# Performance work log

Hardware: AMD Instinct MI355X
Metric: run time of the kernel (lower is better)

## Reference

```python
import jax, jax.numpy as jnp
import numpy as np

B, S, P, N = 256, 128, 100, 500
E, H, L, F = 256, 4, 2, 1024   # embed, heads, layers, ffn
V, U, I = 50000, 10000, 10000


def setup_inputs() -> dict:
    key = jax.random.key(0)
    ks = jax.random.split(key, 32)
    u = lambda k, shp: jax.random.uniform(k, shp, jnp.float32, -0.1, 0.1)
    n = lambda k, shp, s=0.02: jax.random.normal(k, shp, jnp.float32) * s
    inp = {
        'attr': jax.random.randint(ks[0], (B, S), 0, V),
        'attr_inds': jax.random.randint(ks[1], (B, S), 0, S),
        'attr_tf': jax.random.uniform(ks[2], (B, S), jnp.float32),
        'attr_feat': jax.random.normal(ks[3], (B, 13), jnp.float32),
        'attr_lens': jax.random.randint(ks[4], (B,), S // 2, S + 1).at[0].set(S),
        'attr_lens_user': jax.random.randint(ks[5], (B,), 0, S),
        'attr_lens_item': jax.random.randint(ks[6], (B,), 0, S),
        'user_ids': jax.random.randint(ks[7], (B,), 0, U),
        'item_ids': jax.random.randint(ks[8], (B,), 0, I),
        'pos_targets': jax.random.randint(ks[9], (B, P), 0, V),
        'pos_lens': jax.random.randint(ks[10], (B,), 1, P + 1).at[0].set(P),
        'neg_targets': jax.random.randint(ks[11], (B, N), 0, V),
        'neg_lens': jax.random.randint(ks[12], (B,), 1, N + 1).at[0].set(N),
        # parameters (init_uniform(-0.1,0.1) like f_init_weight)
        'attr_emb': u(ks[13], (V, E)),
        'user_emb': u(ks[14], (U, E)),
        'item_emb': u(ks[15], (I, E)),
        'out_emb': u(ks[16], (V, 3 * E)),
        'fw_W': n(ks[17], (1, 13), 0.1),
        'fw_b': jnp.zeros((1,), jnp.float32),
        'qkv_w': n(ks[18], (L, 3 * E, E)),
        'qkv_b': jnp.zeros((L, 3 * E), jnp.float32),
        'attn_out_w': n(ks[19], (L, E, E)),
        'attn_out_b': jnp.zeros((L, E), jnp.float32),
        'ln1_s': jnp.ones((L, E), jnp.float32),
        'ln1_b': jnp.zeros((L, E), jnp.float32),
        'ff1_w': n(ks[20], (L, F, E)),
        'ff1_b': jnp.zeros((L, F), jnp.float32),
        'ff2_w': n(ks[21], (L, E, F)),
        'ff2_b': jnp.zeros((L, E), jnp.float32),
        'ln2_s': jnp.ones((L, E), jnp.float32),
        'ln2_b': jnp.zeros((L, E), jnp.float32),
    }
    return inp


def _ln(x, s, b, eps=1e-5):
    m = jnp.mean(x, axis=-1, keepdims=True)
    v = jnp.mean(jnp.square(x - m), axis=-1, keepdims=True)
    return (x - m) * jax.lax.rsqrt(v + eps) * s + b


def _encoder_layer(x, pad, p):
    # PyTorch TransformerEncoderLayer (post-norm, relu, dropout=0/eval)
    b, s, e = x.shape
    hd = e // H
    qkv = x @ p['qkv_w'].T + p['qkv_b']                      # [B,S,3E]
    q, k, v = jnp.split(qkv, 3, axis=-1)
    q = q.reshape(b, s, H, hd)
    k = k.reshape(b, s, H, hd)
    v = v.reshape(b, s, H, hd)
    scores = jnp.einsum('bqhd,bkhd->bhqk', q, k) / jnp.sqrt(jnp.float32(hd))
    scores = scores + jnp.where(pad[:, None, None, :], -1e9, 0.0)
    a = jax.nn.softmax(scores, axis=-1)
    o = jnp.einsum('bhqk,bkhd->bqhd', a, v).reshape(b, s, e)
    o = o @ p['attn_out_w'].T + p['attn_out_b']
    x = _ln(x + o, p['ln1_s'], p['ln1_b'])
    h = jax.nn.relu(x @ p['ff1_w'].T + p['ff1_b'])
    h = h @ p['ff2_w'].T + p['ff2_b']
    return _ln(x + h, p['ln2_s'], p['ln2_b'])


def reference(attr, attr_inds, attr_tf, attr_feat, attr_lens, attr_lens_user,
              attr_lens_item, user_ids, item_ids, pos_targets, pos_lens,
              neg_targets, neg_lens, attr_emb, user_emb, item_emb, out_emb,
              fw_W, fw_b, qkv_w, qkv_b, attn_out_w, attn_out_b, ln1_s, ln1_b,
              ff1_w, ff1_b, ff2_w, ff2_b, ln2_s, ln2_b):
    b, s = attr.shape
    pos = jnp.arange(s)
    pad = pos[None, :] >= attr_lens[:, None]                 # True = padding
    x = attr_emb[attr]                                       # [B,S,E]
    for l in range(qkv_w.shape[0]):
        p = {'qkv_w': qkv_w[l], 'qkv_b': qkv_b[l],
             'attn_out_w': attn_out_w[l], 'attn_out_b': attn_out_b[l],
             'ln1_s': ln1_s[l], 'ln1_b': ln1_b[l],
             'ff1_w': ff1_w[l], 'ff1_b': ff1_b[l],
             'ff2_w': ff2_w[l], 'ff2_b': ff2_b[l],
             'ln2_s': ln2_s[l], 'ln2_b': ln2_b[l]}
        x = _encoder_layer(x, pad, p)
    # per-sample scalar user weight; vectorized ragged user/item tf weighting
    w_user = jax.nn.sigmoid(attr_feat @ fw_W.T + fw_b)[:, 0]           # [B]
    side = jnp.where(pos[None, :] < attr_lens_user[:, None],
                     w_user[:, None], 1.0 - w_user[:, None])           # [B,S]
    weight = attr_tf * side * (~pad)                                   # [B,S]
    attr_x = jnp.einsum('bs,bse->be', weight, x)                       # [B,E]
    output = jnp.concatenate([user_emb[user_ids], attr_x,
                              item_emb[item_ids]], axis=-1)            # [B,3E]
    pos_logits = jnp.einsum('bpe,be->bp', out_emb[pos_targets], output)
    neg_logits = jnp.einsum('bne,be->bn', out_emb[neg_targets], output)
    pos_valid = jnp.arange(pos_targets.shape[1])[None, :] < pos_lens[:, None]
    neg_valid = jnp.arange(neg_targets.shape[1])[None, :] < neg_lens[:, None]
    logits = jnp.concatenate([pos_logits, neg_logits], axis=-1)
    mask = jnp.concatenate([pos_valid, neg_valid], axis=-1)
    new_targets = jnp.concatenate([jnp.ones_like(pos_targets),
                                   jnp.zeros_like(neg_targets)], axis=1)
    new_targets = new_targets * mask.astype(new_targets.dtype)
    return logits, mask, new_targets
```

## Files before the change

### kernel.cpp

```cpp
#include <hip/hip_runtime.h>
#include <hip/hip_bf16.h>

typedef __bf16 bf16_t;
typedef __bf16 bf16x8 __attribute__((ext_vector_type(8)));
typedef __bf16 bf16x4 __attribute__((ext_vector_type(4)));
typedef float f32x4 __attribute__((ext_vector_type(4)));

#define B_ 256
#define S_ 128
#define E_ 256
#define H_ 4
#define HD_ 64
#define F_ 1024
#define TPOS_ 100
#define TNEG_ 500
#define TT_ 600
#define ROWS_ (B_ * S_)

__global__ __launch_bounds__(256) void cvtall_kernel(
        const float* __restrict__ sq, const float* __restrict__ sa,
        const float* __restrict__ s1, const float* __restrict__ s2,
        bf16_t* __restrict__ dq, bf16_t* __restrict__ da,
        bf16_t* __restrict__ d1, bf16_t* __restrict__ d2) {
    int i = blockIdx.x * 256 + threadIdx.x;
    if (i < 393216) { dq[i] = (bf16_t)sq[i]; }
    else if (i < 524288) { int j = i - 393216; da[j] = (bf16_t)sa[j]; }
    else if (i < 1048576) { int j = i - 524288; d1[j] = (bf16_t)s1[j]; }
    else { int j = i - 1048576; d2[j] = (bf16_t)s2[j]; }
}

__global__ __launch_bounds__(256) void embed_kernel(const int* __restrict__ attr,
        const float* __restrict__ emb, bf16_t* __restrict__ xb) {
    int row = blockIdx.x * 4 + (threadIdx.x >> 6);
    int lane = threadIdx.x & 63;
    int idx = attr[row];
    float4 v = reinterpret_cast<const float4*>(emb + (size_t)idx * E_)[lane];
    bf16x4 o; o[0] = (bf16_t)v.x; o[1] = (bf16_t)v.y; o[2] = (bf16_t)v.z; o[3] = (bf16_t)v.w;
    *reinterpret_cast<bf16x4*>(xb + (size_t)row * E_ + lane * 4) = o;
}

template<bool RELU>
__global__ __launch_bounds__(256) void gemm_kernel(
        const bf16_t* __restrict__ A, const bf16_t* __restrict__ W,
        const float* __restrict__ bias, bf16_t* __restrict__ outB, int M, int N, int K) {
    __shared__ bf16_t lA[2][128 * 32];
    __shared__ bf16_t lB[2][128 * 32];
    int tid = threadIdx.x;
    int wave = tid >> 6, lane = tid & 63;
    int wr = wave >> 1, wc = wave & 1;
    int mBase = blockIdx.y * 128;
    int nBase = blockIdx.x * 128;
    int r16 = lane & 15, kg = lane >> 4;

    int srow = wave * 16 + (lane >> 2);
    int scol = (lane & 3) * 8;
    const bf16_t* gA = A + (size_t)(mBase + srow) * K + scol;
    const bf16_t* gB = W + (size_t)(nBase + srow) * K + scol;
    int ldst = wave * 512;

    f32x4 acc[4][4] = {};

    #define STAGE(buf, k0) { \
        _Pragma("unroll") \
        for (int iss = 0; iss < 2; iss++) { \
            __builtin_amdgcn_global_load_lds( \
                (const __attribute__((address_space(1))) void*)(gA + (size_t)iss * 64 * K + (k0)), \
                (__attribute__((address_space(3))) void*)(&lA[buf][iss * 2048 + ldst]), 16, 0, 0); \
            __builtin_amdgcn_global_load_lds( \
                (const __attribute__((address_space(1))) void*)(gB + (size_t)iss * 64 * K + (k0)), \
                (__attribute__((address_space(3))) void*)(&lB[buf][iss * 2048 + ldst]), 16, 0, 0); \
        } }

    STAGE(0, 0);
    int cur = 0;
    for (int k0 = 0; k0 < K; k0 += 32) {
        __syncthreads();
        if (k0 + 32 < K) STAGE(cur ^ 1, k0 + 32);
        bf16x8 a[4], b[4];
        #pragma unroll
        for (int i = 0; i < 4; i++) {
            a[i] = *reinterpret_cast<const bf16x8*>(&lA[cur][(wr * 64 + i * 16 + r16) * 32 + kg * 8]);
            b[i] = *reinterpret_cast<const bf16x8*>(&lB[cur][(wc * 64 + i * 16 + r16) * 32 + kg * 8]);
        }
        #pragma unroll
        for (int mi = 0; mi < 4; mi++)
            #pragma unroll
            for (int ni = 0; ni < 4; ni++)
                acc[mi][ni] = __builtin_amdgcn_mfma_f32_16x16x32_bf16(a[mi], b[ni], acc[mi][ni], 0, 0, 0);
        cur ^= 1;
    }
    #undef STAGE

    #pragma unroll
    for (int mi = 0; mi < 4; mi++) {
        #pragma unroll
        for (int ni = 0; ni < 4; ni++) {
            int col = nBase + wc * 64 + ni * 16 + r16;
            float bv = bias[col];
            #pragma unroll
            for (int j = 0; j < 4; j++) {
                int row = mBase + wr * 64 + mi * 16 + kg * 4 + j;
                float v = acc[mi][ni][j] + bv;
                if (RELU) v = v > 0.f ? v : 0.f;
                outB[(size_t)row * N + col] = (bf16_t)v;
            }
        }
    }
}

__global__ __launch_bounds__(256) void gemm_ln_kernel(
        const bf16_t* __restrict__ A, const bf16_t* __restrict__ W,
        const float* __restrict__ bias, const float* __restrict__ sc,
        const float* __restrict__ bi, bf16_t* __restrict__ xb, int M, int K) {
    __shared__ bf16_t lA[2][64 * 32];
    __shared__ bf16_t lB[2][256 * 32];
    __shared__ float psum[64][2][2];
    int tid = threadIdx.x;
    int wave = tid >> 6, lane = tid & 63;
    int wm = wave >> 1, wn = wave & 1;
    int mBase = blockIdx.x * 64;
    int r16 = lane & 15, kg = lane >> 4;

    const bf16_t* gA = A + (size_t)(mBase + wave * 16 + (lane >> 2)) * K + (lane & 3) * 8;
    const bf16_t* gB = W + (size_t)((lane >> 2)) * K + (lane & 3) * 8;

    f32x4 acc[2][8] = {};

    #define STAGE2(buf, k0) { \
        __builtin_amdgcn_global_load_lds( \
            (const __attribute__((address_space(1))) void*)(gA + (k0)), \
            (__attribute__((address_space(3))) void*)(&lA[buf][wave * 512]), 16, 0, 0); \
        _Pragma("unroll") \
        for (int iss = 0; iss < 4; iss++) { \
            int q = wave * 4 + iss; \
            __builtin_amdgcn_global_load_lds( \
                (const __attribute__((address_space(1))) void*)(gB + (size_t)q * 16 * K + (k0)), \
                (__attribute__((address_space(3))) void*)(&lB[buf][q * 512]), 16, 0, 0); \
        } }

    STAGE2(0, 0);
    int cur = 0;
    for (int k0 = 0; k0 < K; k0 += 32) {
        __syncthreads();
        if (k0 + 32 < K) STAGE2(cur ^ 1, k0 + 32);
        bf16x8 a[2], b[8];
        #pragma unroll
        for (int mi = 0; mi < 2; mi++)
            a[mi] = *reinterpret_cast<const bf16x8*>(&lA[cur][(wm * 32 + mi * 16 + r16) * 32 + kg * 8]);
        #pragma unroll
        for (int ni = 0; ni < 8; ni++)
            b[ni] = *reinterpret_cast<const bf16x8*>(&lB[cur][(wn * 128 + ni * 16 + r16) * 32 + kg * 8]);
        #pragma unroll
        for (int mi = 0; mi < 2; mi++)
            #pragma unroll
            for (int ni = 0; ni < 8; ni++)
                acc[mi][ni] = __builtin_amdgcn_mfma_f32_16x16x32_bf16(a[mi], b[ni], acc[mi][ni], 0, 0, 0);
        cur ^= 1;
    }
    #undef STAGE2

    float bv[8];
    #pragma unroll
    for (int ni = 0; ni < 8; ni++) bv[ni] = bias[wn * 128 + ni * 16 + r16];
    #pragma unroll
    for (int mi = 0; mi < 2; mi++) {
        #pragma unroll
        for (int j = 0; j < 4; j++) {
            int rl = wm * 32 + mi * 16 + kg * 4 + j;
            const bf16_t* rrow = xb + (size_t)(mBase + rl) * 256;
            float s = 0.f, q = 0.f;
            #pragma unroll
            for (int ni = 0; ni < 8; ni++) {
                int col = wn * 128 + ni * 16 + r16;
                float v = acc[mi][ni][j] + bv[ni] + (float)rrow[col];
                acc[mi][ni][j] = v;
                s += v; q += v * v;
            }
            #pragma unroll
            for (int m = 1; m < 16; m <<= 1) { s += __shfl_xor(s, m); q += __shfl_xor(q, m); }
            if (r16 == 0) { psum[rl][wn][0] = s; psum[rl][wn][1] = q; }
        }
    }
    __syncthreads();
    #pragma unroll
    for (int mi = 0; mi < 2; mi++) {
        #pragma unroll
        for (int j = 0; j < 4; j++) {
            int rl = wm * 32 + mi * 16 + kg * 4 + j;
            float s = psum[rl][0][0] + psum[rl][1][0];
            float qq = psum[rl][0][1] + psum[rl][1][1];
            float mean = s * (1.0f / 256.0f);
            float var = qq * (1.0f / 256.0f) - mean * mean;
            float inv = rsqrtf(var + 1e-5f);
            bf16_t* orow = xb + (size_t)(mBase + rl) * 256;
            #pragma unroll
            for (int ni = 0; ni < 8; ni++) {
                int col = wn * 128 + ni * 16 + r16;
                float o = (acc[mi][ni][j] - mean) * inv * sc[col] + bi[col];
                orow[col] = (bf16_t)o;
            }
        }
    }
}

__global__ __launch_bounds__(256) void attn_kernel(const bf16_t* __restrict__ qkv,
        const int* __restrict__ lens, bf16_t* __restrict__ out) {
    __shared__ bf16_t p[S_][S_ + 8];
    __shared__ bf16_t vl[HD_][S_ + 8];
    int bh = blockIdx.x; int b = bh >> 2, h = bh & 3;
    int wave = threadIdx.x >> 6, lane = threadIdx.x & 63;
    int r16 = lane & 15, kg = lane >> 4;
    int q0 = wave * 32;
    int len = lens[b];
    const bf16_t* qbase = qkv + (size_t)b * S_ * 768;

    {
        int sl = (wave & 1) * 64 + lane;
        const bf16_t* vsrc = qbase + (size_t)sl * 768 + 512 + h * HD_;
        #pragma unroll
        for (int pass = 0; pass < 4; pass++) {
            int d0 = (pass * 2 + (wave >> 1)) * 8;
            bf16x8 v = *reinterpret_cast<const bf16x8*>(vsrc + d0);
            #pragma unroll
            for (int j = 0; j < 8; j++) vl[d0 + j][sl] = v[j];
        }
    }

    f32x4 acc[2][8] = {};
    #pragma unroll
    for (int ks = 0; ks < 2; ks++) {
        int kOff = h * HD_ + ks * 32 + kg * 8;
        bf16x8 a[2], bb[8];
        #pragma unroll
        for (int mi = 0; mi < 2; mi++)
            a[mi] = *reinterpret_cast<const bf16x8*>(qbase + (size_t)(q0 + mi * 16 + r16) * 768 + kOff);
        #pragma unroll
        for (int ni = 0; ni < 8; ni++)
            bb[ni] = *reinterpret_cast<const bf16x8*>(qbase + (size_t)(ni * 16 + r16) * 768 + 256 + kOff);
        #pragma unroll
        for (int mi = 0; mi < 2; mi++)
            #pragma unroll
            for (int ni = 0; ni < 8; ni++)
                acc[mi][ni] = __builtin_amdgcn_mfma_f32_16x16x32_bf16(a[mi], bb[ni], acc[mi][ni], 0, 0, 0);
    }
    #pragma unroll
    for (int mi = 0; mi < 2; mi++) {
        #pragma unroll
        for (int j = 0; j < 4; j++) {
            float vals[8]; float mx = -1e30f;
            #pragma unroll
            for (int ni = 0; ni < 8; ni++) {
                int kp = ni * 16 + r16;
                float v = acc[mi][ni][j] * 0.125f;
                vals[ni] = (kp < len) ? v : -1e30f;
                mx = fmaxf(mx, vals[ni]);
            }
            #pragma unroll
            for (int m = 1; m < 16; m <<= 1) mx = fmaxf(mx, __shfl_xor(mx, m));
            float sum = 0.f;
            #pragma unroll
            for (int ni = 0; ni < 8; ni++) {
                vals[ni] = (vals[ni] > -1e29f) ? __expf(vals[ni] - mx) : 0.f;
                sum += vals[ni];
            }
            #pragma unroll
            for (int m = 1; m < 16; m <<= 1) sum += __shfl_xor(sum, m);
            float inv = 1.0f / sum;
            int row = q0 + mi * 16 + kg * 4 + j;
            #pragma unroll
            for (int ni = 0; ni < 8; ni++)
                p[row][ni * 16 + r16] = (bf16_t)(vals[ni] * inv);
        }
    }
    __syncthreads();
    f32x4 acc2[2][4] = {};
    #pragma unroll
    for (int ks = 0; ks < 4; ks++) {
        int k = ks * 32 + kg * 8;
        bf16x8 a[2], bb[4];
        #pragma unroll
        for (int mi = 0; mi < 2; mi++)
            a[mi] = *reinterpret_cast<const bf16x8*>(&p[q0 + mi * 16 + r16][k]);
        #pragma unroll
        for (int ni = 0; ni < 4; ni++)
            bb[ni] = *reinterpret_cast<const bf16x8*>(&vl[ni * 16 + r16][k]);
        #pragma unroll
        for (int mi = 0; mi < 2; mi++)
            #pragma unroll
            for (int ni = 0; ni < 4; ni++)
                acc2[mi][ni] = __builtin_amdgcn_mfma_f32_16x16x32_bf16(a[mi], bb[ni], acc2[mi][ni], 0, 0, 0);
    }
    #pragma unroll
    for (int mi = 0; mi < 2; mi++)
        #pragma unroll
        for (int ni = 0; ni < 4; ni++)
            #pragma unroll
            for (int j = 0; j < 4; j++) {
                int q = q0 + mi * 16 + kg * 4 + j;
                int d = ni * 16 + r16;
                out[((size_t)b * S_ + q) * E_ + h * HD_ + d] = (bf16_t)acc2[mi][ni][j];
            }
}

__global__ void wuser_kernel(const float* __restrict__ feat, const float* __restrict__ W,
                             const float* __restrict__ bb, float* __restrict__ wu) {
    int b = threadIdx.x;
    if (b < B_) {
        float z = bb[0];
        #pragma unroll
        for (int i = 0; i < 13; i++) z += feat[b * 13 + i] * W[i];
        wu[b] = 1.f / (1.f + __expf(-z));
    }
}

__global__ __launch_bounds__(256) void pool_kernel(
        const bf16_t* __restrict__ xb, const float* __restrict__ attr_tf,
        const int* __restrict__ lens, const int* __restrict__ lens_user,
        const float* __restrict__ wu, const int* __restrict__ uid, const int* __restrict__ iid,
        const float* __restrict__ user_emb, const float* __restrict__ item_emb,
        float* __restrict__ outvec) {
    int b = blockIdx.x, t = threadIdx.x;
    __shared__ float wrow[S_];
    if (t < S_) {
        float w = (t < lens[b]) ? attr_tf[b * S_ + t] : 0.f;
        float side = (t < lens_user[b]) ? wu[b] : (1.f - wu[b]);
        wrow[t] = w * side;
    }
    __syncthreads();
    float acc = 0.f;
    const bf16_t* xr = xb + (size_t)b * S_ * E_ + t;
    #pragma unroll 4
    for (int s = 0; s < S_; s++) acc += wrow[s] * (float)xr[(size_t)s * E_];
    outvec[b * 768 + 256 + t] = acc;
    outvec[b * 768 + t] = user_emb[(size_t)uid[b] * E_ + t];
    outvec[b * 768 + 512 + t] = item_emb[(size_t)iid[b] * E_ + t];
}

__global__ __launch_bounds__(256) void logits_kernel(
        const float* __restrict__ outvec, const float* __restrict__ out_emb,
        const int* __restrict__ pos_t, const int* __restrict__ pos_l,
        const int* __restrict__ neg_t, const int* __restrict__ neg_l,
        float* __restrict__ dout) {
    int gg = blockIdx.x * 4 + (threadIdx.x >> 6);
    int lane = threadIdx.x & 63;
    int b = gg / (TT_ / 2);
    int u = gg - b * (TT_ / 2);
    int pl = pos_l[b], nl = neg_l[b];
    int t0 = u * 2, t1 = u * 2 + 1;

    int tgt0, tgt1, valid0, valid1, ispos0, ispos1;
    if (t0 < TPOS_) { tgt0 = pos_t[b * TPOS_ + t0]; valid0 = (t0 < pl); ispos0 = 1; }
    else { int tn = t0 - TPOS_; tgt0 = neg_t[b * TNEG_ + tn]; valid0 = (tn < nl); ispos0 = 0; }
    if (t1 < TPOS_) { tgt1 = pos_t[b * TPOS_ + t1]; valid1 = (t1 < pl); ispos1 = 1; }
    else { int tn = t1 - TPOS_; tgt1 = neg_t[b * TNEG_ + tn]; valid1 = (tn < nl); ispos1 = 0; }

    const float4* e0 = reinterpret_cast<const float4*>(out_emb + (size_t)tgt0 * 768);
    const float4* e1 = reinterpret_cast<const float4*>(out_emb + (size_t)tgt1 * 768);
    const float4* o4 = reinterpret_cast<const float4*>(outvec + (size_t)b * 768);
    float acc0 = 0.f, acc1 = 0.f;
    #pragma unroll
    for (int c = 0; c < 3; c++) {
        float4 a0 = e0[c * 64 + lane];
        float4 a1 = e1[c * 64 + lane];
        float4 o = o4[c * 64 + lane];
        acc0 += a0.x * o.x + a0.y * o.y + a0.z * o.z + a0.w * o.w;
        acc1 += a1.x * o.x + a1.y * o.y + a1.z * o.z + a1.w * o.w;
    }
    #pragma unroll
    for (int m = 1; m < 64; m <<= 1) { acc0 += __shfl_xor(acc0, m); acc1 += __shfl_xor(acc1, m); }
    if (lane == 0) {
        size_t i0 = (size_t)b * TT_ + t0;
        dout[i0] = acc0;
        dout[i0 + 1] = acc1;
        dout[(size_t)B_ * TT_ + i0] = valid0 ? 1.0f : 0.0f;
        dout[(size_t)B_ * TT_ + i0 + 1] = valid1 ? 1.0f : 0.0f;
        dout[2 * (size_t)B_ * TT_ + i0] = (valid0 && ispos0) ? 1.0f : 0.0f;
        dout[2 * (size_t)B_ * TT_ + i0 + 1] = (valid1 && ispos1) ? 1.0f : 0.0f;
    }
}

extern "C" void kernel_launch(void* const* d_in, const int* in_sizes, int n_in,
                              void* d_out, int out_size, void* d_ws, size_t ws_size,
                              hipStream_t stream) {
    const int*   attr        = (const int*)d_in[0];
    const float* attr_tf     = (const float*)d_in[2];
    const float* attr_feat   = (const float*)d_in[3];
    const int*   attr_lens   = (const int*)d_in[4];
    const int*   attr_lens_u = (const int*)d_in[5];
    const int*   user_ids    = (const int*)d_in[7];
    const int*   item_ids    = (const int*)d_in[8];
    const int*   pos_targets = (const int*)d_in[9];
    const int*   pos_lens    = (const int*)d_in[10];
    const int*   neg_targets = (const int*)d_in[11];
    const int*   neg_lens    = (const int*)d_in[12];
    const float* attr_emb    = (const float*)d_in[13];
    const float* user_emb    = (const float*)d_in[14];
    const float* item_emb    = (const float*)d_in[15];
    const float* out_emb     = (const float*)d_in[16];
    const float* fw_W        = (const float*)d_in[17];
    const float* fw_b        = (const float*)d_in[18];
    const float* qkv_w       = (const float*)d_in[19];
    const float* qkv_b       = (const float*)d_in[20];
    const float* attn_out_w  = (const float*)d_in[21];
    const float* attn_out_b  = (const float*)d_in[22];
    const float* ln1_s       = (const float*)d_in[23];
    const float* ln1_b       = (const float*)d_in[24];
    const float* ff1_w       = (const float*)d_in[25];
    const float* ff1_b       = (const float*)d_in[26];
    const float* ff2_w       = (const float*)d_in[27];
    const float* ff2_b       = (const float*)d_in[28];
    const float* ln2_s       = (const float*)d_in[29];
    const float* ln2_b       = (const float*)d_in[30];

    size_t szRes = (size_t)ROWS_ * E_ * 2;
    size_t wB = (size_t)1572864 * 2;
    size_t fixedB = 2 * szRes + wB + (size_t)B_ * 768 * 4 + 4096 + 16384;
    int CH = 32;
    for (int ch = 1; ch <= 32; ch <<= 1) {
        if (fixedB + (size_t)(ROWS_ / ch) * 1024 * 2 <= ws_size) { CH = ch; break; }
    }
    int rowsC = ROWS_ / CH, sampC = B_ / CH;

    char* ws = (char*)d_ws;
    size_t off = 0;
    auto alloc = [&](size_t bytes) { void* pp = ws + off; off += (bytes + 255) & ~255ULL; return pp; };
    bf16_t* xb  = (bf16_t*)alloc(szRes);
    bf16_t* ob  = (bf16_t*)alloc(szRes);
    bf16_t* wq  = (bf16_t*)alloc((size_t)393216 * 2);
    bf16_t* wa  = (bf16_t*)alloc((size_t)131072 * 2);
    bf16_t* w1  = (bf16_t*)alloc((size_t)524288 * 2);
    bf16_t* w2  = (bf16_t*)alloc((size_t)524288 * 2);
    float* outvec = (float*)alloc((size_t)B_ * 768 * 4);
    float* wu     = (float*)alloc(1024);
    bf16_t* chunk = (bf16_t*)alloc((size_t)rowsC * 1024 * 2);

    cvtall_kernel<<<6144, 256, 0, stream>>>(qkv_w, attn_out_w, ff1_w, ff2_w, wq, wa, w1, w2);
    embed_kernel<<<ROWS_ / 4, 256, 0, stream>>>(attr, attr_emb, xb);

    for (int l = 0; l < 2; l++) {
        for (int c = 0; c < CH; c++) {
            size_t r0 = (size_t)c * rowsC;
            gemm_kernel<false><<<dim3(6, rowsC / 128), 256, 0, stream>>>(
                xb + r0 * E_, wq + (size_t)l * 768 * 256, qkv_b + l * 768, chunk, rowsC, 768, 256);
            attn_kernel<<<sampC * H_, 256, 0, stream>>>(chunk, attr_lens + c * sampC, ob + r0 * E_);
        }
        gemm_ln_kernel<<<ROWS_ / 64, 256, 0, stream>>>(
            ob, wa + (size_t)l * 256 * 256, attn_out_b + l * 256,
            ln1_s + l * 256, ln1_b + l * 256, xb, ROWS_, 256);
        for (int c = 0; c < CH; c++) {
            size_t r0 = (size_t)c * rowsC;
            gemm_kernel<true><<<dim3(8, rowsC / 128), 256, 0, stream>>>(
                xb + r0 * E_, w1 + (size_t)l * 1024 * 256, ff1_b + l * 1024, chunk, rowsC, 1024, 256);
            gemm_ln_kernel<<<rowsC / 64, 256, 0, stream>>>(
                chunk, w2 + (size_t)l * 256 * 1024, ff2_b + l * 256,
                ln2_s + l * 256, ln2_b + l * 256, xb + r0 * E_, rowsC, 1024);
        }
    }

    wuser_kernel<<<1, 256, 0, stream>>>(attr_feat, fw_W, fw_b, wu);
    pool_kernel<<<B_, 256, 0, stream>>>(xb, attr_tf, attr_lens, attr_lens_u, wu,
                                        user_ids, item_ids, user_emb, item_emb, outvec);
    logits_kernel<<<B_ * TT_ / 8, 256, 0, stream>>>(outvec, out_emb, pos_targets, pos_lens,
                                                    neg_targets, neg_lens, (float*)d_out);
}
```

Before: 388.9 us.

## Preload full K=256 weight tile into LDS and swizzle LDS layouts in GEMM

The generic GEMM is specialized for K=256. The whole 128x256 weight tile is now loaded into shared memory once at block start, and only the A tile is double-buffered per K step. Both LDS layouts use XOR swizzling to reduce bank conflicts on the bf16x8 fragment reads. LDS use per block rises to about 80KB, which may lower occupancy, and the B preload has to finish before any compute starts.

```diff
diff --git a/kernel.cpp b/kernel.cpp
--- a/kernel.cpp
+++ b/kernel.cpp
@@ -40,11 +40,11 @@
 }
 
 template<bool RELU>
-__global__ __launch_bounds__(256) void gemm_kernel(
+__global__ __launch_bounds__(256) void gemm256_kernel(
         const bf16_t* __restrict__ A, const bf16_t* __restrict__ W,
-        const float* __restrict__ bias, bf16_t* __restrict__ outB, int M, int N, int K) {
+        const float* __restrict__ bias, bf16_t* __restrict__ outB, int M, int N) {
+    __shared__ bf16_t lB[128 * 256];
     __shared__ bf16_t lA[2][128 * 32];
-    __shared__ bf16_t lB[2][128 * 32];
     int tid = threadIdx.x;
     int wave = tid >> 6, lane = tid & 63;
     int wr = wave >> 1, wc = wave & 1;
@@ -52,35 +52,41 @@
     int nBase = blockIdx.x * 128;
     int r16 = lane & 15, kg = lane >> 4;
 
-    int srow = wave * 16 + (lane >> 2);
-    int scol = (lane & 3) * 8;
-    const bf16_t* gA = A + (size_t)(mBase + srow) * K + scol;
-    const bf16_t* gB = W + (size_t)(nBase + srow) * K + scol;
-    int ldst = wave * 512;
-
-    f32x4 acc[4][4] = {};
-
-    #define STAGE(buf, k0) { \
+    #pragma unroll
+    for (int j = 0; j < 16; j++) {
+        int s = j * 256 + tid;
+        int row = s >> 5, pc = s & 31;
+        int sc = pc ^ (row & 7);
+        __builtin_amdgcn_global_load_lds(
+            (const __attribute__((address_space(1))) void*)(W + (size_t)(nBase + row) * 256 + sc * 8),
+            (__attribute__((address_space(3))) void*)(&lB[(j * 4 + wave) * 512]), 16, 0, 0);
+    }
+
+    #define STAGEA(buf, k0) { \
         _Pragma("unroll") \
         for (int iss = 0; iss < 2; iss++) { \
+            int s = iss * 256 + tid; \
+            int row = s >> 2, pc = s & 3; \
+            int sc = pc ^ (row & 3); \
             __builtin_amdgcn_global_load_lds( \
-                (const __attribute__((address_space(1))) void*)(gA + (size_t)iss * 64 * K + (k0)), \
-                (__attribute__((address_space(3))) void*)(&lA[buf][iss * 2048 + ldst]), 16, 0, 0); \
-            __builtin_amdgcn_global_load_lds( \
-                (const __attribute__((address_space(1))) void*)(gB + (size_t)iss * 64 * K + (k0)), \
-                (__attribute__((address_space(3))) void*)(&lB[buf][iss * 2048 + ldst]), 16, 0, 0); \
+                (const __attribute__((address_space(1))) void*)(A + (size_t)(mBase + row) * 256 + (k0) + sc * 8), \
+                (__attribute__((address_space(3))) void*)(&lA[buf][iss * 2048 + wave * 512]), 16, 0, 0); \
         } }
 
-    STAGE(0, 0);
+    f32x4 acc[4][4] = {};
+    STAGEA(0, 0);
     int cur = 0;
-    for (int k0 = 0; k0 < K; k0 += 32) {
+    for (int k0 = 0; k0 < 256; k0 += 32) {
         __syncthreads();
-        if (k0 + 32 < K) STAGE(cur ^ 1, k0 + 32);
+        if (k0 + 32 < 256) STAGEA(cur ^ 1, k0 + 32);
+        int cB = k0 >> 3;
         bf16x8 a[4], b[4];
         #pragma unroll
         for (int i = 0; i < 4; i++) {
-            a[i] = *reinterpret_cast<const bf16x8*>(&lA[cur][(wr * 64 + i * 16 + r16) * 32 + kg * 8]);
-            b[i] = *reinterpret_cast<const bf16x8*>(&lB[cur][(wc * 64 + i * 16 + r16) * 32 + kg * 8]);
+            int ra = wr * 64 + i * 16 + r16;
+            a[i] = *reinterpret_cast<const bf16x8*>(&lA[cur][ra * 32 + (kg ^ (ra & 3)) * 8]);
+            int rb = wc * 64 + i * 16 + r16;
+            b[i] = *reinterpret_cast<const bf16x8*>(&lB[rb * 256 + ((cB + kg) ^ (rb & 7)) * 8]);
         }
         #pragma unroll
         for (int mi = 0; mi < 4; mi++)
@@ -89,7 +95,7 @@
                 acc[mi][ni] = __builtin_amdgcn_mfma_f32_16x16x32_bf16(a[mi], b[ni], acc[mi][ni], 0, 0, 0);
         cur ^= 1;
     }
-    #undef STAGE
+    #undef STAGEA
 
     #pragma unroll
     for (int mi = 0; mi < 4; mi++) {
@@ -440,8 +446,8 @@
     for (int l = 0; l < 2; l++) {
         for (int c = 0; c < CH; c++) {
             size_t r0 = (size_t)c * rowsC;
-            gemm_kernel<false><<<dim3(6, rowsC / 128), 256, 0, stream>>>(
-                xb + r0 * E_, wq + (size_t)l * 768 * 256, qkv_b + l * 768, chunk, rowsC, 768, 256);
+            gemm256_kernel<false><<<dim3(6, rowsC / 128), 256, 0, stream>>>(
+                xb + r0 * E_, wq + (size_t)l * 768 * 256, qkv_b + l * 768, chunk, rowsC, 768);
             attn_kernel<<<sampC * H_, 256, 0, stream>>>(chunk, attr_lens + c * sampC, ob + r0 * E_);
         }
         gemm_ln_kernel<<<ROWS_ / 64, 256, 0, stream>>>(
@@ -449,8 +455,8 @@
             ln1_s + l * 256, ln1_b + l * 256, xb, ROWS_, 256);
         for (int c = 0; c < CH; c++) {
             size_t r0 = (size_t)c * rowsC;
-            gemm_kernel<true><<<dim3(8, rowsC / 128), 256, 0, stream>>>(
-                xb + r0 * E_, w1 + (size_t)l * 1024 * 256, ff1_b + l * 1024, chunk, rowsC, 1024, 256);
+            gemm256_kernel<true><<<dim3(8, rowsC / 128), 256, 0, stream>>>(
+                xb + r0 * E_, w1 + (size_t)l * 1024 * 256, ff1_b + l * 1024, chunk, rowsC, 1024);
             gemm_ln_kernel<<<rowsC / 64, 256, 0, stream>>>(
                 chunk, w2 + (size_t)l * 256 * 1024, ff2_b + l * 256,
                 ln2_s + l * 256, ln2_b + l * 256, xb + r0 * E_, rowsC, 1024);
```

New measurement: 391.3 us (median of 2 runs). About the same (+0.6%).
